# Optimization experiments

Measured on AMD Instinct MI355X. Metric: run time of the kernel, lower is better.

The kernel has to match this reference:

```python
import jax, jax.numpy as jnp
import numpy as np

HEAD_SIZE = 128
EMBED_DIM = 1024
BLOCK = 2048


def setup_inputs() -> dict:
    key = jax.random.key(0)
    kx, kk, kq, kv = jax.random.split(key, 4)
    x = jax.random.normal(kx, (8, BLOCK, EMBED_DIM), dtype=jnp.float32)
    # nn.Linear weights stored as [out, in]; apply as x @ W.T -> keep as [in, out]
    s = 1.0 / np.sqrt(EMBED_DIM)
    W_key = jax.random.uniform(kk, (EMBED_DIM, HEAD_SIZE), jnp.float32, -s, s)
    W_query = jax.random.uniform(kq, (EMBED_DIM, HEAD_SIZE), jnp.float32, -s, s)
    W_value = jax.random.uniform(kv, (EMBED_DIM, HEAD_SIZE), jnp.float32, -s, s)
    return {"x": x, "W_key": W_key, "W_query": W_query, "W_value": W_value}


def reference(x, W_key, W_query, W_value):
    # NOTE: faithful to the source bug: q = self.key(x), W_query is unused.
    B, T, C = x.shape
    k = x @ W_key          # [B, T, H]
    q = x @ W_key          # [B, T, H]  (source uses key() for q too)
    scores = jnp.einsum("bqh,bkh->bqk", q, k) * (HEAD_SIZE ** -0.5)
    causal = jnp.tril(jnp.ones((T, T), dtype=bool))
    scores = jnp.where(causal, scores, -jnp.inf)
    weights = jax.nn.softmax(scores, axis=-1)
    v = x @ W_value        # [B, T, H]
    out = jnp.einsum("bqk,bkh->bqh", weights, v)
    return out
```

## Files before the change

### kernel.cpp

```cpp
#include <hip/hip_runtime.h>
#include <hip/hip_bf16.h>

typedef __attribute__((ext_vector_type(8))) short bf16x8;
typedef __attribute__((ext_vector_type(4))) short bf16x4;
typedef __attribute__((ext_vector_type(4))) float f32x4;

#define HS 128
#define ED 1024
#define TT 2048
#define NBATCH 8
#define NROWS (NBATCH * TT)
#define CHUNKS 4
#define TPC 8

__device__ __forceinline__ short bf16rne(float f) {
    unsigned u = __builtin_bit_cast(unsigned, f);
    u = u + 0x7fffu + ((u >> 16) & 1u);
    return (short)(u >> 16);
}

template <int N>
__device__ __forceinline__ void vmwait() {
    if constexpr (N == 0)      asm volatile("s_waitcnt vmcnt(0)" ::: "memory");
    else if constexpr (N == 4) asm volatile("s_waitcnt vmcnt(4)" ::: "memory");
    else                       asm volatile("s_waitcnt vmcnt(8)" ::: "memory");
}
__device__ __forceinline__ void lds_barrier() {
    asm volatile("s_waitcnt lgkmcnt(0)" ::: "memory");
    __builtin_amdgcn_s_barrier();
}

__device__ __forceinline__ void gl_lds16(const void* g, void* l) {
    __builtin_amdgcn_global_load_lds(
        (const __attribute__((address_space(1))) unsigned int*)g,
        (__attribute__((address_space(3))) unsigned int*)l, 16, 0, 0);
}

template <int NCALLS, int RBL2>
__device__ __forceinline__ void stage_tile(const char* gbase, void* lds,
                                           int gpitch, int tid, int wv) {
#pragma unroll
    for (int c = 0; c < NCALLS; ++c) {
        const int o = c * 4096 + tid * 16;
        const int row = o >> RBL2;
        const int colU = (o & ((1 << RBL2) - 1)) ^ ((row & 7) << 4);
        const char* g = gbase + (size_t)row * gpitch + colU;
        char* l = (char*)lds + c * 4096 + wv * 1024;
        gl_lds16(g, l);
    }
}

__device__ __forceinline__ bf16x8 lds_rd7(const short* lds, int row, int colE) {
    const int o = (row << 7) + (((colE * 2) & 127) ^ ((row & 7) << 4));
    return *reinterpret_cast<const bf16x8*>((const char*)lds + o);
}
__device__ __forceinline__ bf16x8 lds_rd8(const short* lds, int row, int colE) {
    const int o = (row << 8) + (((colE * 2) & 255) ^ ((row & 7) << 4));
    return *reinterpret_cast<const bf16x8*>((const char*)lds + o);
}

__global__ void k_wtrans(const float* __restrict__ Wk, const float* __restrict__ Wv,
                         short* __restrict__ WkT, short* __restrict__ WvT) {
    const float* W = blockIdx.y ? Wv : Wk;
    short* WT = blockIdx.y ? WvT : WkT;
    __shared__ float tile[16][128];
    const int k0 = blockIdx.x * 16;
    const int t = threadIdx.x;
#pragma unroll
    for (int i = 0; i < 8; ++i) {
        int idx = t + i * 256;
        tile[idx >> 7][idx & 127] = W[(size_t)(k0 + (idx >> 7)) * HS + (idx & 127)];
    }
    __syncthreads();
    const int n = t >> 1;
    const int h = (t & 1) * 8;
    bf16x8 o;
#pragma unroll
    for (int i = 0; i < 8; ++i) o[i] = bf16rne(tile[h + i][n]);
    *reinterpret_cast<bf16x8*>(&WT[(size_t)n * ED + k0 + h]) = o;
}

__global__ __launch_bounds__(256) void k_proj(
        const float* __restrict__ x,
        const short* __restrict__ WkT, const short* __restrict__ WvT,
        short* __restrict__ Kbuf, short* __restrict__ VT) {
    __shared__ short xl[2][64 * 64];
    __shared__ short wl[2][128 * 64];

    const int tid = threadIdx.x;
    const int lane = tid & 63;
    const int wv = tid >> 6;
    const int lr = lane & 15, g = lane >> 4;
    const int side = blockIdx.x;
    const int r0 = blockIdx.y * 64;
    const short* WT = side ? WvT : WkT;

    f32x4 acc[8];
#pragma unroll
    for (int i = 0; i < 8; ++i) acc[i] = (f32x4){0.f, 0.f, 0.f, 0.f};

    int xo[2], xrow[2], xcolU[2];
#pragma unroll
    for (int j = 0; j < 2; ++j) {
        xo[j] = tid * 32 + j * 16;
        xrow[j] = xo[j] >> 7;
        xcolU[j] = (xo[j] & 127) ^ ((xrow[j] & 7) << 4);
    }
    f32x4 xr[2][2][2];

#define XLOAD(s, set)                                                                \
    {                                                                                \
        _Pragma("unroll") for (int j = 0; j < 2; ++j) {                              \
            const float* sp = x + (size_t)(r0 + xrow[j]) * ED + (s) * 64 + (xcolU[j] >> 1); \
            xr[set][j][0] = *reinterpret_cast<const f32x4*>(sp);                     \
            xr[set][j][1] = *reinterpret_cast<const f32x4*>(sp + 4);                 \
        }                                                                            \
    }
#define XWRITE(set, buf)                                                             \
    {                                                                                \
        _Pragma("unroll") for (int j = 0; j < 2; ++j) {                              \
            bf16x8 pk;                                                               \
            _Pragma("unroll") for (int i = 0; i < 8; ++i)                            \
                pk[i] = bf16rne(xr[set][j][i >> 2][i & 3]);                          \
            *reinterpret_cast<bf16x8*>((char*)&xl[buf][0] + xo[j]) = pk;             \
        }                                                                            \
    }

    XLOAD(0, 0);
    XLOAD(1, 1);
    stage_tile<4, 7>((const char*)WT, &wl[0][0], ED * 2, tid, wv);
    vmwait<0>();
    XWRITE(0, 0);
    lds_barrier();

#pragma unroll
    for (int s = 0; s < 16; ++s) {
        if (s + 1 < 16)
            stage_tile<4, 7>((const char*)WT + (size_t)(s + 1) * 128,
                             &wl[(s + 1) & 1][0], ED * 2, tid, wv);
        if (s + 2 < 16) XLOAD(s + 2, s & 1);
        bf16x8 af[2];
#pragma unroll
        for (int ks = 0; ks < 2; ++ks)
            af[ks] = lds_rd7(&xl[s & 1][0], wv * 16 + lr, ks * 32 + g * 8);
#pragma unroll
        for (int ks = 0; ks < 2; ++ks)
#pragma unroll
            for (int nf = 0; nf < 8; ++nf) {
                bf16x8 bfr = lds_rd7(&wl[s & 1][0], nf * 16 + lr, ks * 32 + g * 8);
                acc[nf] = __builtin_amdgcn_mfma_f32_16x16x32_bf16(af[ks], bfr, acc[nf], 0, 0, 0);
            }
        if (s + 2 < 16) vmwait<4>();
        else            vmwait<0>();
        if (s + 1 < 16) XWRITE((s + 1) & 1, (s + 1) & 1);
        lds_barrier();
    }
#undef XLOAD
#undef XWRITE

    const int mb = r0 + wv * 16 + 4 * g;
    if (side == 0) {
#pragma unroll
        for (int nf = 0; nf < 8; ++nf) {
            const int n = nf * 16 + lr;
#pragma unroll
            for (int r = 0; r < 4; ++r)
                Kbuf[(size_t)(mb + r) * HS + n] = bf16rne(acc[nf][r]);
        }
    } else {
        const int b = mb >> 11, tt = mb & (TT - 1);
#pragma unroll
        for (int nf = 0; nf < 8; ++nf) {
            const int n = nf * 16 + lr;
            bf16x4 o;
#pragma unroll
            for (int r = 0; r < 4; ++r) o[r] = bf16rne(acc[nf][r]);
            *reinterpret_cast<bf16x4*>(&VT[((size_t)b * HS + n) * TT + tt]) = o;
        }
    }
}

__global__ __launch_bounds__(256) void k_attn(
        const short* __restrict__ Kbuf, const short* __restrict__ VT,
        float* __restrict__ Opart, float* __restrict__ ml) {
    __shared__ short kl[2][64 * 128];
    __shared__ short vl[2][128 * 64];
    __shared__ short plds[4][16][72];

    const int tid = threadIdx.x;
    const int lane = tid & 63;
    const int wv = tid >> 6;
    const int lr = lane & 15, g = lane >> 4;

    const int bid = blockIdx.x;
    const int b = bid & 7;
    const int w = bid >> 3;
    int c, qt;
    if (w < 32)      { c = 0; qt = 31 - w; }
    else if (w < 56) { c = 1; qt = 31 - (w - 32); }
    else if (w < 72) { c = 2; qt = 31 - (w - 56); }
    else             { c = 3; qt = 31 - (w - 72); }
    const int t_begin = c * TPC;
    const int t_end = min(t_begin + TPC, qt + 1);

    const short* Kb = Kbuf + (size_t)b * TT * HS;
    const short* Vb = VT + (size_t)b * HS * TT;
    const int q0 = qt * 64 + wv * 16;

    bf16x8 qf[4];
#pragma unroll
    for (int ks = 0; ks < 4; ++ks)
        qf[ks] = *reinterpret_cast<const bf16x8*>(&Kb[(size_t)(q0 + lr) * HS + ks * 32 + g * 8]);

    stage_tile<4, 8>((const char*)(Kb + (size_t)t_begin * 64 * HS), &kl[0][0], HS * 2, tid, wv);
    stage_tile<4, 7>((const char*)(Vb + t_begin * 64), &vl[0][0], TT * 2, tid, wv);

    float mrun = -1e30f, lrun = 0.f;
    f32x4 oacc[8];
#pragma unroll
    for (int i = 0; i < 8; ++i) oacc[i] = (f32x4){0.f, 0.f, 0.f, 0.f};

    const float c1 = 0.08838834764831845f * 1.4426950408889634f;
    const int qrow = q0 + lr;

    for (int t = t_begin; t < t_end; ++t) {
        const int bi = (t - t_begin) & 1;
        if (t + 1 < t_end) {
            stage_tile<4, 8>((const char*)(Kb + (size_t)(t + 1) * 64 * HS), &kl[bi ^ 1][0],
                             HS * 2, tid, wv);
            stage_tile<4, 7>((const char*)(Vb + (t + 1) * 64), &vl[bi ^ 1][0], TT * 2, tid, wv);
            vmwait<8>();
        } else {
            vmwait<0>();
        }
        __builtin_amdgcn_s_barrier();

        const int kv0 = t * 64;
        f32x4 s[4];
#pragma unroll
        for (int i = 0; i < 4; ++i) s[i] = (f32x4){0.f, 0.f, 0.f, 0.f};
        __builtin_amdgcn_s_setprio(1);
#pragma unroll
        for (int ks = 0; ks < 4; ++ks) {
            bf16x8 kf[4];
#pragma unroll
            for (int mf = 0; mf < 4; ++mf)
                kf[mf] = lds_rd8(&kl[bi][0], mf * 16 + lr, ks * 32 + g * 8);
#pragma unroll
            for (int mf = 0; mf < 4; ++mf)
                s[mf] = __builtin_amdgcn_mfma_f32_16x16x32_bf16(kf[mf], qf[ks], s[mf], 0, 0, 0);
        }
        __builtin_amdgcn_s_setprio(0);

        float pv[4][4];
        float tmax = -1e30f;
#pragma unroll
        for (int mf = 0; mf < 4; ++mf)
#pragma unroll
            for (int r = 0; r < 4; ++r) {
                const int kv = kv0 + mf * 16 + 4 * g + r;
                float v = s[mf][r] * c1;
                v = (kv <= qrow) ? v : -1e30f;
                pv[mf][r] = v;
                tmax = fmaxf(tmax, v);
            }
        tmax = fmaxf(tmax, __shfl_xor(tmax, 16));
        tmax = fmaxf(tmax, __shfl_xor(tmax, 32));
        const float mnew = fmaxf(mrun, tmax);
        const float alpha = exp2f(mrun - mnew);
        mrun = mnew;
        float tsum = 0.f;
#pragma unroll
        for (int mf = 0; mf < 4; ++mf)
#pragma unroll
            for (int r = 0; r < 4; ++r) {
                const float p = exp2f(pv[mf][r] - mnew);
                pv[mf][r] = p;
                tsum += p;
            }
        tsum += __shfl_xor(tsum, 16);
        tsum += __shfl_xor(tsum, 32);
        lrun = lrun * alpha + tsum;
#pragma unroll
        for (int i = 0; i < 8; ++i) oacc[i] *= alpha;

#pragma unroll
        for (int mf = 0; mf < 4; ++mf) {
            bf16x4 pk;
#pragma unroll
            for (int r = 0; r < 4; ++r) pk[r] = bf16rne(pv[mf][r]);
            *reinterpret_cast<bf16x4*>(&plds[wv][lr][mf * 16 + g * 4]) = pk;
        }
        __builtin_amdgcn_s_setprio(1);
#pragma unroll
        for (int ks = 0; ks < 2; ++ks) {
            bf16x8 pf = *reinterpret_cast<const bf16x8*>(&plds[wv][lr][ks * 32 + g * 8]);
            bf16x8 vf[8];
#pragma unroll
            for (int mf = 0; mf < 8; ++mf)
                vf[mf] = lds_rd7(&vl[bi][0], mf * 16 + lr, ks * 32 + g * 8);
#pragma unroll
            for (int mf = 0; mf < 8; ++mf)
                oacc[mf] = __builtin_amdgcn_mfma_f32_16x16x32_bf16(vf[mf], pf, oacc[mf], 0, 0, 0);
        }
        __builtin_amdgcn_s_setprio(0);

        lds_barrier();
    }

    const int row = b * TT + q0 + lr;
    const size_t pidx = (size_t)c * NROWS + row;
    float* op = Opart + pidx * HS;
#pragma unroll
    for (int mf = 0; mf < 8; ++mf)
        *reinterpret_cast<f32x4*>(&op[mf * 16 + g * 4]) = oacc[mf];
    if (lane < 16) {
        ml[pidx * 2] = mrun;
        ml[pidx * 2 + 1] = lrun;
    }
}

__global__ __launch_bounds__(256) void k_merge(const float* __restrict__ Opart,
                                               const float* __restrict__ ml,
                                               float* __restrict__ out) {
    const int idx = blockIdx.x * 256 + threadIdx.x;
    const int row = idx >> 5;
    const int h4 = (idx & 31) * 4;
    const int qt64 = (row & (TT - 1)) >> 6;
    const int nvalid = (qt64 >> 3) + 1;
    float m[CHUNKS], l[CHUNKS];
    float M = -1e30f;
#pragma unroll
    for (int c = 0; c < CHUNKS; ++c) {
        const bool valid = c < nvalid;
        const size_t p = (size_t)c * NROWS + row;
        m[c] = valid ? ml[p * 2] : -1e30f;
        l[c] = valid ? ml[p * 2 + 1] : 0.f;
        M = fmaxf(M, m[c]);
    }
    float denom = 0.f;
    f32x4 o = (f32x4){0.f, 0.f, 0.f, 0.f};
#pragma unroll
    for (int c = 0; c < CHUNKS; ++c) {
        const bool valid = c < nvalid;
        const float wgt = valid ? exp2f(m[c] - M) : 0.f;
        denom += wgt * l[c];
        if (valid) {
            f32x4 p = *reinterpret_cast<const f32x4*>(
                &Opart[((size_t)c * NROWS + row) * HS + h4]);
            o += p * wgt;
        }
    }
    const float inv = 1.0f / denom;
    *reinterpret_cast<f32x4*>(&out[(size_t)row * HS + h4]) = o * inv;
}

extern "C" void kernel_launch(void* const* d_in, const int* in_sizes, int n_in,
                              void* d_out, int out_size, void* d_ws, size_t ws_size,
                              hipStream_t stream) {
    (void)in_sizes; (void)n_in; (void)out_size; (void)ws_size;
    const float* x  = (const float*)d_in[0];
    const float* Wk = (const float*)d_in[1];
    const float* Wv = (const float*)d_in[3];
    float* out = (float*)d_out;

    char* ws = (char*)d_ws;
    short* Kbuf = (short*)ws;
    short* VT   = (short*)(ws + (size_t)NROWS * HS * 2);
    short* WkT  = (short*)(ws + 2 * (size_t)NROWS * HS * 2);
    short* WvT  = WkT + (size_t)HS * ED;
    float* Opart = (float*)(WvT + (size_t)HS * ED);
    float* mlb   = Opart + (size_t)CHUNKS * NROWS * HS;

    hipLaunchKernelGGL(k_wtrans, dim3(64, 2), dim3(256), 0, stream, Wk, Wv, WkT, WvT);
    hipLaunchKernelGGL(k_proj, dim3(2, NROWS / 64), dim3(256), 0, stream, x, WkT, WvT, Kbuf, VT);
    hipLaunchKernelGGL(k_attn, dim3(640), dim3(256), 0, stream, Kbuf, VT, Opart, mlb);
    hipLaunchKernelGGL(k_merge, dim3(NROWS * 32 / 256), dim3(256), 0, stream, Opart, mlb, out);
}
```

Baseline: 165.3 us.

## Load x straight into MFMA registers and store attention partials as bf16

The projection kernel now reads x directly into the per-lane A-fragment layout and converts it to bf16 in registers. This drops the x staging buffer in LDS and its write and read traffic. The weight tiles move to a three-stage LDS ring, fetched two steps ahead. The attention kernel now writes its per-chunk partial outputs as bf16 instead of fp32, and the merge kernel reads them back as bf16, which halves that intermediate traffic at some cost in precision.

```diff
diff --git a/kernel.cpp b/kernel.cpp
--- a/kernel.cpp
+++ b/kernel.cpp
@@ -18,6 +18,10 @@
     u = u + 0x7fffu + ((u >> 16) & 1u);
     return (short)(u >> 16);
 }
+__device__ __forceinline__ float bf16tof(short s) {
+    unsigned u = ((unsigned)(unsigned short)s) << 16;
+    return __builtin_bit_cast(float, u);
+}
 
 template <int N>
 __device__ __forceinline__ void vmwait() {
@@ -84,8 +88,7 @@
         const float* __restrict__ x,
         const short* __restrict__ WkT, const short* __restrict__ WvT,
         short* __restrict__ Kbuf, short* __restrict__ VT) {
-    __shared__ short xl[2][64 * 64];
-    __shared__ short wl[2][128 * 64];
+    __shared__ short wl[3][128 * 64];
 
     const int tid = threadIdx.x;
     const int lane = tid & 63;
@@ -94,71 +97,61 @@
     const int side = blockIdx.x;
     const int r0 = blockIdx.y * 64;
     const short* WT = side ? WvT : WkT;
+    const int m0 = r0 + wv * 16;
 
     f32x4 acc[8];
 #pragma unroll
     for (int i = 0; i < 8; ++i) acc[i] = (f32x4){0.f, 0.f, 0.f, 0.f};
 
-    int xo[2], xrow[2], xcolU[2];
-#pragma unroll
-    for (int j = 0; j < 2; ++j) {
-        xo[j] = tid * 32 + j * 16;
-        xrow[j] = xo[j] >> 7;
-        xcolU[j] = (xo[j] & 127) ^ ((xrow[j] & 7) << 4);
-    }
+    const float* xbase = x + (size_t)(m0 + lr) * ED + g * 8;
     f32x4 xr[2][2][2];
 
-#define XLOAD(s, set)                                                                \
-    {                                                                                \
-        _Pragma("unroll") for (int j = 0; j < 2; ++j) {                              \
-            const float* sp = x + (size_t)(r0 + xrow[j]) * ED + (s) * 64 + (xcolU[j] >> 1); \
-            xr[set][j][0] = *reinterpret_cast<const f32x4*>(sp);                     \
-            xr[set][j][1] = *reinterpret_cast<const f32x4*>(sp + 4);                 \
-        }                                                                            \
-    }
-#define XWRITE(set, buf)                                                             \
-    {                                                                                \
-        _Pragma("unroll") for (int j = 0; j < 2; ++j) {                              \
-            bf16x8 pk;                                                               \
-            _Pragma("unroll") for (int i = 0; i < 8; ++i)                            \
-                pk[i] = bf16rne(xr[set][j][i >> 2][i & 3]);                          \
-            *reinterpret_cast<bf16x8*>((char*)&xl[buf][0] + xo[j]) = pk;             \
-        }                                                                            \
+#define XLOAD(s, set)                                                          \
+    {                                                                          \
+        _Pragma("unroll") for (int ks = 0; ks < 2; ++ks) {                     \
+            const float* sp = xbase + (s) * 64 + ks * 32;                      \
+            xr[set][ks][0] = *reinterpret_cast<const f32x4*>(sp);              \
+            xr[set][ks][1] = *reinterpret_cast<const f32x4*>(sp + 4);          \
+        }                                                                      \
+    }
+#define XCVT(set, af)                                                          \
+    {                                                                          \
+        _Pragma("unroll") for (int ks = 0; ks < 2; ++ks)                       \
+            _Pragma("unroll") for (int i = 0; i < 8; ++i)                      \
+                af[ks][i] = bf16rne(xr[set][ks][i >> 2][i & 3]);               \
     }
 
     XLOAD(0, 0);
     XLOAD(1, 1);
     stage_tile<4, 7>((const char*)WT, &wl[0][0], ED * 2, tid, wv);
-    vmwait<0>();
-    XWRITE(0, 0);
+    stage_tile<4, 7>((const char*)WT + 128, &wl[1][0], ED * 2, tid, wv);
+    vmwait<4>();
     lds_barrier();
 
 #pragma unroll
     for (int s = 0; s < 16; ++s) {
-        if (s + 1 < 16)
-            stage_tile<4, 7>((const char*)WT + (size_t)(s + 1) * 128,
-                             &wl[(s + 1) & 1][0], ED * 2, tid, wv);
-        if (s + 2 < 16) XLOAD(s + 2, s & 1);
         bf16x8 af[2];
+        XCVT(s & 1, af);
+        if (s + 2 < 16) {
+            XLOAD(s + 2, s & 1);
+            stage_tile<4, 7>((const char*)WT + (size_t)(s + 2) * 128,
+                             &wl[(s + 2) % 3][0], ED * 2, tid, wv);
+        }
 #pragma unroll
         for (int ks = 0; ks < 2; ++ks)
-            af[ks] = lds_rd7(&xl[s & 1][0], wv * 16 + lr, ks * 32 + g * 8);
-#pragma unroll
-        for (int ks = 0; ks < 2; ++ks)
 #pragma unroll
             for (int nf = 0; nf < 8; ++nf) {
-                bf16x8 bfr = lds_rd7(&wl[s & 1][0], nf * 16 + lr, ks * 32 + g * 8);
+                bf16x8 bfr = lds_rd7(&wl[s % 3][0], nf * 16 + lr, ks * 32 + g * 8);
                 acc[nf] = __builtin_amdgcn_mfma_f32_16x16x32_bf16(af[ks], bfr, acc[nf], 0, 0, 0);
             }
-        if (s + 2 < 16) vmwait<4>();
+        if (s + 2 < 16) vmwait<8>();
         else            vmwait<0>();
-        if (s + 1 < 16) XWRITE((s + 1) & 1, (s + 1) & 1);
         lds_barrier();
     }
 #undef XLOAD
-#undef XWRITE
-
-    const int mb = r0 + wv * 16 + 4 * g;
+#undef XCVT
+
+    const int mb = m0 + 4 * g;
     if (side == 0) {
 #pragma unroll
         for (int nf = 0; nf < 8; ++nf) {
@@ -182,7 +175,7 @@
 
 __global__ __launch_bounds__(256) void k_attn(
         const short* __restrict__ Kbuf, const short* __restrict__ VT,
-        float* __restrict__ Opart, float* __restrict__ ml) {
+        short* __restrict__ Opart, float* __restrict__ ml) {
     __shared__ short kl[2][64 * 128];
     __shared__ short vl[2][128 * 64];
     __shared__ short plds[4][16][72];
@@ -310,17 +303,21 @@
 
     const int row = b * TT + q0 + lr;
     const size_t pidx = (size_t)c * NROWS + row;
-    float* op = Opart + pidx * HS;
-#pragma unroll
-    for (int mf = 0; mf < 8; ++mf)
-        *reinterpret_cast<f32x4*>(&op[mf * 16 + g * 4]) = oacc[mf];
+    short* op = Opart + pidx * HS;
+#pragma unroll
+    for (int mf = 0; mf < 8; ++mf) {
+        bf16x4 ob;
+#pragma unroll
+        for (int r = 0; r < 4; ++r) ob[r] = bf16rne(oacc[mf][r]);
+        *reinterpret_cast<bf16x4*>(&op[mf * 16 + g * 4]) = ob;
+    }
     if (lane < 16) {
         ml[pidx * 2] = mrun;
         ml[pidx * 2 + 1] = lrun;
     }
 }
 
-__global__ __launch_bounds__(256) void k_merge(const float* __restrict__ Opart,
+__global__ __launch_bounds__(256) void k_merge(const short* __restrict__ Opart,
                                                const float* __restrict__ ml,
                                                float* __restrict__ out) {
     const int idx = blockIdx.x * 256 + threadIdx.x;
@@ -346,9 +343,10 @@
         const float wgt = valid ? exp2f(m[c] - M) : 0.f;
         denom += wgt * l[c];
         if (valid) {
-            f32x4 p = *reinterpret_cast<const f32x4*>(
+            bf16x4 pb = *reinterpret_cast<const bf16x4*>(
                 &Opart[((size_t)c * NROWS + row) * HS + h4]);
-            o += p * wgt;
+#pragma unroll
+            for (int j = 0; j < 4; ++j) o[j] += wgt * bf16tof(pb[j]);
         }
     }
     const float inv = 1.0f / denom;
@@ -369,8 +367,8 @@
     short* VT   = (short*)(ws + (size_t)NROWS * HS * 2);
     short* WkT  = (short*)(ws + 2 * (size_t)NROWS * HS * 2);
     short* WvT  = WkT + (size_t)HS * ED;
-    float* Opart = (float*)(WvT + (size_t)HS * ED);
-    float* mlb   = Opart + (size_t)CHUNKS * NROWS * HS;
+    short* Opart = WvT + (size_t)HS * ED;
+    float* mlb   = (float*)(Opart + (size_t)CHUNKS * NROWS * HS);
 
     hipLaunchKernelGGL(k_wtrans, dim3(64, 2), dim3(256), 0, stream, Wk, Wv, WkT, WvT);
     hipLaunchKernelGGL(k_proj, dim3(2, NROWS / 64), dim3(256), 0, stream, x, WkT, WvT, Kbuf, VT);
```

Result: no change. 162.7 us (-1.6%).
